# Kernel tuning notes

Measured on AMD Instinct MI355X. Metric: run time of the kernel, lower is better.

Reference implementation:

```python
import jax, jax.numpy as jnp
import numpy as np

B, S, HOPS, DIM, NREL = 1024, 32, 2, 64, 237
NENT, NEDGE = 14541, 272115
SIGMA = 0.1
CFMW = 64


def setup_inputs() -> dict:
    key = jax.random.key(0)
    ks = jax.random.split(key, 20)

    def g(k, shape):
        return (jax.random.normal(k, shape, dtype=jnp.float32) / np.float32(np.sqrt(shape[0])))

    inp = {
        "entity_pairs": jax.random.randint(ks[0], (B, 2), 0, NENT),
        "train_edges": jax.random.randint(ks[1], (B,), 0, NEDGE),
        "labels": jax.random.randint(ks[2], (B,), 0, NREL),
        "entity2edges": jax.random.randint(ks[3], (NENT + 1, S), 0, NEDGE + 1),
        "edge2entities": jax.random.randint(ks[4], (NEDGE + 1, 1), 0, NENT + 1),
        "edge2relation": jax.random.randint(ks[5], (NEDGE + 1,), 0, NREL + 1),
        "t": jax.random.uniform(ks[6], (B,), dtype=jnp.float32),
        "eps": jax.random.normal(ks[7], (B, NREL), dtype=jnp.float32),
        "rel_feat": g(ks[8], (NREL, DIM)),
        "W_agg0": g(ks[9], (DIM, DIM)), "b_agg0": jnp.zeros((DIM,), jnp.float32),
        "W_agg1": g(ks[10], (DIM, NREL)), "b_agg1": jnp.zeros((NREL,), jnp.float32),
        "W_out": g(ks[11], (2 * NREL, NREL)), "b_out": jnp.zeros((NREL,), jnp.float32),
        "mW1": g(ks[12], (NREL + 1, CFMW)), "mb1": jnp.zeros((CFMW,), jnp.float32),
        "mW2": g(ks[13], (CFMW, CFMW)), "mb2": jnp.zeros((CFMW,), jnp.float32),
        "mW3": g(ks[14], (CFMW, CFMW)), "mb3": jnp.zeros((CFMW,), jnp.float32),
        "mW4": g(ks[15], (CFMW, NREL)), "mb4": jnp.zeros((NREL,), jnp.float32),
    }
    return inp


def _side(ent, labels, train_edges, entity2edges, edge2entities, edge2relation, relf, aggs):
    # multi-hop neighbor edge gather + masks (exclude the training edge itself)
    edges_list = [labels]  # hop-0 "edges" are the relation labels
    masks = []
    for i in range(HOPS):
        if i == 0:
            ne = ent.reshape(B, 1)  # (B, 1) source entities
        else:
            ne = edge2entities[edges_list[-1].reshape(-1)].reshape(B, -1)
        nedges = entity2edges[ne.reshape(-1)].reshape(B, -1)  # (B, S**(i+1))
        edges_list.append(nedges)
        masks.append((nedges != train_edges[:, None]).astype(relf.dtype))
    # edge -> relation -> feature
    ev = [relf[edges_list[0]]]  # (B, DIM)
    for edges in edges_list[1:]:
        ev.append(relf[edge2relation[edges]])  # (B, S**h, DIM)
    # iterative mean aggregation (PathCon-style, one entity per edge)
    for i in range(HOPS):
        W, b, act, self_inc = aggs[i]
        d = W.shape[0]
        nxt = []
        for hop in range(HOPS - i):
            neigh = ev[hop + 1].reshape(B, -1, 1, S, d)
            m = masks[hop].reshape(B, -1, 1, S, 1)
            out = jnp.mean(jnp.mean(neigh * m, axis=-2), axis=-2)  # (B, S**hop, d)
            if self_inc:
                out = out + ev[hop].reshape(B, -1, d)
            nxt.append(act(out @ W + b))
        ev = nxt
    return ev[0].reshape(B, NREL)


def reference(entity_pairs, train_edges, labels, entity2edges, edge2entities,
              edge2relation, t, eps, rel_feat, W_agg0, b_agg0, W_agg1, b_agg1,
              W_out, b_out, mW1, mb1, mW2, mb2, mW3, mb3, mW4, mb4):
    relf = jnp.concatenate([rel_feat, jnp.zeros((1, DIM), rel_feat.dtype)], axis=0)
    aggs = [
        (W_agg0, b_agg0, jax.nn.relu, True),    # intermediate hop: relu, self-included
        (W_agg1, b_agg1, lambda x: x, False),   # last hop: identity, no self
    ]
    x0 = _side(entity_pairs[:, 0], labels, train_edges, entity2edges,
               edge2entities, edge2relation, relf, aggs)
    x1 = _side(entity_pairs[:, 1], labels, train_edges, entity2edges,
               edge2entities, edge2relation, relf, aggs)
    output = jnp.concatenate([x0, x1], axis=-1) @ W_out + b_out  # (B, NREL)
    # CFM: xt = (1-t) x0 + t x1 + sigma*eps ; ut = x1 - x0
    tb = t[:, None]
    xt = (1.0 - tb) * x0 + tb * x1 + SIGMA * eps
    h = jnp.concatenate([xt, tb], axis=-1)
    h = jax.nn.selu(h @ mW1 + mb1)
    h = jax.nn.selu(h @ mW2 + mb2)
    h = jax.nn.selu(h @ mW3 + mb3)
    vt = h @ mW4 + mb4
    scores = output * vt
    return scores
```

## Files before the change

kernel.cpp:

```cpp
#include <hip/hip_runtime.h>
#include <math.h>

#define BB 1024
#define S 32
#define DIM 64
#define NREL 237
#define SIGMA 0.1f

#define OFS_WR    0
#define N_WR      (238*64)
#define OFS_WC0   (OFS_WR + N_WR)
#define N_WC      (64*237)
#define OFS_WC1   (OFS_WC0 + N_WC)
#define OFS_BC    (OFS_WC1 + N_WC)
#define OFS_HC    (OFS_BC + 237)

#define LDS_BYTES 76288

__device__ __forceinline__ float selu_f(float x) {
    const float alpha = 1.6732632423543772f;
    const float scale = 1.0507009873554805f;
    return scale * (x > 0.f ? x : alpha * expm1f(x));
}

__global__ __launch_bounds__(256) void precompute_kernel(
    const float* __restrict__ rel_feat, const float* __restrict__ W0,
    const float* __restrict__ W1, const float* __restrict__ b1,
    const float* __restrict__ W_out, const float* __restrict__ b_out,
    const float* __restrict__ mW1, const float* __restrict__ mb1,
    float* __restrict__ ws) {
    __shared__ float red[256];
    int blk = blockIdx.x;
    const int tid = threadIdx.x;

    if (blk < 60) {
        int idx = blk * 256 + tid;
        if (idx < 238 * 64) {
            int r = idx >> 6, o = idx & 63;
            float acc = 0.f;
            if (r < NREL) {
#pragma unroll 8
                for (int d = 0; d < 64; ++d)
                    acc += rel_feat[r * 64 + d] * W0[d * 64 + o];
            }
            ws[OFS_WR + idx] = acc;
        }
        return;
    }
    blk -= 60;
    if (blk < 512) {
        int half = blk >> 8;
        int lb = blk & 255;
        int o = lb >> 2, ct = lb & 3;
        int cl = tid & 63, g = tid >> 6;
        int c = ct * 64 + cl;
        const float* Wsrc = W_out + half * 237 * 237;
        float acc = 0.f;
        if (c < NREL) {
            int k0 = g * 60, k1 = (g == 3) ? 237 : (k0 + 60);
#pragma unroll 4
            for (int k = k0; k < k1; ++k)
                acc += W1[o * 237 + k] * Wsrc[k * 237 + c];
        }
        red[tid] = acc;
        __syncthreads();
        if (g == 0 && c < NREL) {
            float s = red[cl] + red[64 + cl] + red[128 + cl] + red[192 + cl];
            ws[(half ? OFS_WC1 : OFS_WC0) + o * 237 + c] = s;
        }
        return;
    }
    blk -= 512;
    if (blk < 4) {
        int cl = tid & 63, g = tid >> 6;
        int c = blk * 64 + cl;
        float acc = 0.f;
        if (c < NREL) {
            int k0 = g * 60, k1 = (g == 3) ? 237 : (k0 + 60);
#pragma unroll 4
            for (int k = k0; k < k1; ++k)
                acc += b1[k] * (W_out[k * 237 + c] + W_out[(237 + k) * 237 + c]);
        }
        red[tid] = acc;
        __syncthreads();
        if (g == 0 && c < NREL)
            ws[OFS_BC + c] = b_out[c] + red[cl] + red[64 + cl] + red[128 + cl] + red[192 + cl];
        return;
    }
    {
        int w = tid & 63, g = tid >> 6;
        int k0 = g * 60, k1 = (g == 3) ? 237 : (k0 + 60);
        float acc = 0.f;
#pragma unroll 4
        for (int k = k0; k < k1; ++k)
            acc += b1[k] * mW1[k * 64 + w];
        red[tid] = acc;
        __syncthreads();
        if (g == 0)
            ws[OFS_HC + w] = mb1[w] + red[w] + red[64 + w] + red[128 + w] + red[192 + w];
    }
}

__global__ __launch_bounds__(512) void gf_kernel(
    const int* __restrict__ ep, const int* __restrict__ te_arr,
    const int* __restrict__ e2e_tab, const int* __restrict__ e2ent,
    const int* __restrict__ e2r, const float* __restrict__ b0,
    const float* __restrict__ t_arr, const float* __restrict__ eps,
    const float* __restrict__ W1, const float* __restrict__ mW1,
    const float* __restrict__ mW2, const float* __restrict__ mb2,
    const float* __restrict__ mW3, const float* __restrict__ mb3,
    const float* __restrict__ mW4, const float* __restrict__ mb4,
    const float* __restrict__ ws, float* __restrict__ out) {
    extern __shared__ float smem[];
    float* s_wr   = smem;
    int*   s_r2m  = (int*)(smem + 15232);
    int*   s_r1   = (int*)(smem + 16256);
    int*   s_ent2 = (int*)(smem + 16384);
    float* s_m1   = smem + 16512;
    float* s_v1   = smem + 16640;
    float* s_ov   = smem + 18816;

    const int tid = threadIdx.x;
    const int bb = blockIdx.x * 2;
    const int g = tid >> 4;
    const int c = tid & 15;
    const int te0 = te_arr[bb];
    const int te1 = te_arr[bb + 1];
    const float4 b0v = ((const float4*)b0)[c];

    {
        const float4* src = (const float4*)(ws + OFS_WR);
        float4* dst = (float4*)s_wr;
        for (int i = tid; i < 238 * 16; i += 512) dst[i] = src[i];
    }
    const float4* sWr4 = (const float4*)s_wr;

    if (tid < 128) {
        int u = tid >> 5, s = tid & 31;
        int b = bb + (u >> 1), side = u & 1;
        int te = (u >> 1) ? te1 : te0;
        int ent = ep[b * 2 + side];
        int e1 = e2e_tab[ent * S + s];
        s_r1[u * 32 + s] = e2r[e1];
        s_m1[u * 32 + s] = (e1 != te) ? 1.0f : 0.0f;
        s_ent2[u * 32 + s] = e2ent[e1];
    }
    __syncthreads();

    for (int p = tid; p < 1024; p += 512) {
        int j = p >> 5, s = p & 31;
        int e2 = e2e_tab[s_ent2[j] * S + s];
        s_r2m[p] = (e2 == te0) ? NREL : e2r[e2];
    }
    __syncthreads();

    const float inv = 1.0f / 32.0f;
    for (int u = 0; u < 4; ++u) {
        {
            const int j = g;
            const int* rr = &s_r2m[j * 32];
            float4 acc = sWr4[s_r1[u * 32 + j] * 16 + c];
            float4 sa = make_float4(0.f, 0.f, 0.f, 0.f);
            float4 sb = make_float4(0.f, 0.f, 0.f, 0.f);
#pragma unroll
            for (int s = 0; s < 16; ++s) {
                float4 v = sWr4[rr[s] * 16 + c];
                sa.x += v.x; sa.y += v.y; sa.z += v.z; sa.w += v.w;
            }
#pragma unroll
            for (int s = 16; s < 32; ++s) {
                float4 v = sWr4[rr[s] * 16 + c];
                sb.x += v.x; sb.y += v.y; sb.z += v.z; sb.w += v.w;
            }
            float m = s_m1[u * 32 + j];
            float4 r;
            r.x = fmaxf(acc.x + (sa.x + sb.x) * inv + b0v.x, 0.f) * m;
            r.y = fmaxf(acc.y + (sa.y + sb.y) * inv + b0v.y, 0.f) * m;
            r.z = fmaxf(acc.z + (sa.z + sb.z) * inv + b0v.z, 0.f) * m;
            r.w = fmaxf(acc.w + (sa.w + sb.w) * inv + b0v.w, 0.f) * m;
            *((float4*)&s_v1[j * 68 + c * 4]) = r;
        }
        __syncthreads();
        if (tid < 64) {
            float sum = 0.f;
#pragma unroll 8
            for (int j = 0; j < 32; ++j) sum += s_v1[j * 68 + tid];
            s_ov[u * 64 + tid] = sum * inv;
        }
        if (u < 3) {
            const int un = u + 1;
            const int te = (un >> 1) ? te1 : te0;
            for (int p = tid; p < 1024; p += 512) {
                int j = p >> 5, s = p & 31;
                int e2 = e2e_tab[s_ent2[un * 32 + j] * S + s];
                s_r2m[p] = (e2 == te) ? NREL : e2r[e2];
            }
        }
        __syncthreads();
    }

    float* s_omix = smem;
    float* s_ymix = smem + 128;
    float* s_outv = smem + 608;
    float* s_red  = smem + 1088;
    float* s_h    = smem + 1600;
    const float* Wc0 = ws + OFS_WC0;
    const float* Wc1 = ws + OFS_WC1;
    const float* bc = ws + OFS_BC;
    const float* hc = ws + OFS_HC;

    const int p  = tid >> 8;
    const int lt = tid & 255;
    const float tb = t_arr[bb + p];

    if (lt < 64) {
        float o0 = s_ov[(p * 2 + 0) * 64 + lt];
        float o1 = s_ov[(p * 2 + 1) * 64 + lt];
        s_omix[p * 64 + lt] = (1.f - tb) * o0 + tb * o1;
    }
    __syncthreads();

    if (lt < NREL) {
        float y = 0.f, a = bc[lt];
#pragma unroll 4
        for (int d = 0; d < 64; ++d) {
            y += s_omix[p * 64 + d] * W1[d * 237 + lt];
            a += s_ov[p * 128 + d] * Wc0[d * 237 + lt]
               + s_ov[p * 128 + 64 + d] * Wc1[d * 237 + lt];
        }
        s_ymix[p * 240 + lt] = y;
        s_outv[p * 240 + lt] = a;
    }
    __syncthreads();

    {
        int w = lt & 63, gg = lt >> 6;
        float a = 0.f;
        int k0 = gg * 60, k1 = (gg == 3) ? 237 : (k0 + 60);
        const float* e = eps + (bb + p) * 237;
#pragma unroll 4
        for (int k = k0; k < k1; ++k)
            a += (SIGMA * e[k] + s_ymix[p * 240 + k]) * mW1[k * 64 + w];
        s_red[p * 256 + lt] = a;
    }
    __syncthreads();
    if (lt < 64) {
        float h = hc[lt] + tb * mW1[237 * 64 + lt]
                + s_red[p * 256 + lt] + s_red[p * 256 + 64 + lt]
                + s_red[p * 256 + 128 + lt] + s_red[p * 256 + 192 + lt];
        s_h[p * 64 + lt] = selu_f(h);
    }
    __syncthreads();

    {
        int w = lt & 63, gg = lt >> 6;
        float a = 0.f;
#pragma unroll
        for (int d = gg * 16; d < gg * 16 + 16; ++d)
            a += s_h[p * 64 + d] * mW2[d * 64 + w];
        s_red[p * 256 + lt] = a;
    }
    __syncthreads();
    if (lt < 64) {
        float v = mb2[lt] + s_red[p * 256 + lt] + s_red[p * 256 + 64 + lt]
                + s_red[p * 256 + 128 + lt] + s_red[p * 256 + 192 + lt];
        s_h[p * 64 + lt] = selu_f(v);
    }
    __syncthreads();

    {
        int w = lt & 63, gg = lt >> 6;
        float a = 0.f;
#pragma unroll
        for (int d = gg * 16; d < gg * 16 + 16; ++d)
            a += s_h[p * 64 + d] * mW3[d * 64 + w];
        s_red[p * 256 + lt] = a;
    }
    __syncthreads();
    if (lt < 64) {
        float v = mb3[lt] + s_red[p * 256 + lt] + s_red[p * 256 + 64 + lt]
                + s_red[p * 256 + 128 + lt] + s_red[p * 256 + 192 + lt];
        s_h[p * 64 + lt] = selu_f(v);
    }
    __syncthreads();

    if (lt < NREL) {
        float a = mb4[lt];
#pragma unroll 4
        for (int w = 0; w < 64; ++w)
            a += s_h[p * 64 + w] * mW4[w * 237 + lt];
        out[(bb + p) * 237 + lt] = s_outv[p * 240 + lt] * a;
    }
}

extern "C" void kernel_launch(void* const* d_in, const int* in_sizes, int n_in,
                              void* d_out, int out_size, void* d_ws, size_t ws_size,
                              hipStream_t stream) {
    const int* ep       = (const int*)d_in[0];
    const int* te       = (const int*)d_in[1];
    const int* e2e      = (const int*)d_in[3];
    const int* e2ent    = (const int*)d_in[4];
    const int* e2r      = (const int*)d_in[5];
    const float* t      = (const float*)d_in[6];
    const float* eps    = (const float*)d_in[7];
    const float* relf   = (const float*)d_in[8];
    const float* W0     = (const float*)d_in[9];
    const float* b0     = (const float*)d_in[10];
    const float* W1     = (const float*)d_in[11];
    const float* b1     = (const float*)d_in[12];
    const float* W_out  = (const float*)d_in[13];
    const float* b_out  = (const float*)d_in[14];
    const float* mW1    = (const float*)d_in[15];
    const float* mb1    = (const float*)d_in[16];
    const float* mW2    = (const float*)d_in[17];
    const float* mb2    = (const float*)d_in[18];
    const float* mW3    = (const float*)d_in[19];
    const float* mb3    = (const float*)d_in[20];
    const float* mW4    = (const float*)d_in[21];
    const float* mb4    = (const float*)d_in[22];
    float* ws  = (float*)d_ws;
    float* out = (float*)d_out;

    hipLaunchKernelGGL(precompute_kernel, dim3(577), dim3(256), 0, stream,
                       relf, W0, W1, b1, W_out, b_out, mW1, mb1, ws);
    hipLaunchKernelGGL(gf_kernel, dim3(BB / 2), dim3(512), LDS_BYTES, stream,
                       ep, te, e2e, e2ent, e2r, b0,
                       t, eps, W1, mW1, mW2, mb2, mW3, mb3, mW4, mb4, ws, out);
}
```

Before: 147.5 us.

## Store relation-weight table as bf16 in LDS and process one sample per block

The precomputed relation×W0 table is now rounded to bf16, which halves its global-to-LDS copy and LDS footprint (about 44KB instead of 76KB). That allows more blocks to be resident per CU. The main kernel now runs one batch row per 512-thread block with 1024 blocks instead of two rows per block. The MLP reductions are rewritten to spread work over all 512 threads with 8-way partial sums. The cost is bf16 rounding error in the aggregated features, and each block still repeats the table load.

```diff
diff --git a/kernel.cpp b/kernel.cpp
--- a/kernel.cpp
+++ b/kernel.cpp
@@ -7,20 +7,23 @@
 #define NREL 237
 #define SIGMA 0.1f
 
-#define OFS_WR    0
-#define N_WR      (238*64)
-#define OFS_WC0   (OFS_WR + N_WR)
+#define OFS_WC0   7616
 #define N_WC      (64*237)
 #define OFS_WC1   (OFS_WC0 + N_WC)
 #define OFS_BC    (OFS_WC1 + N_WC)
 #define OFS_HC    (OFS_BC + 237)
 
-#define LDS_BYTES 76288
+#define LDS_BYTES 44544
 
 __device__ __forceinline__ float selu_f(float x) {
     const float alpha = 1.6732632423543772f;
     const float scale = 1.0507009873554805f;
     return scale * (x > 0.f ? x : alpha * expm1f(x));
+}
+
+__device__ __forceinline__ unsigned short f2bf(float f) {
+    unsigned int b = __float_as_uint(f);
+    return (unsigned short)((b + 0x7fffu + ((b >> 16) & 1u)) >> 16);
 }
 
 __global__ __launch_bounds__(256) void precompute_kernel(
@@ -43,7 +46,7 @@
                 for (int d = 0; d < 64; ++d)
                     acc += rel_feat[r * 64 + d] * W0[d * 64 + o];
             }
-            ws[OFS_WR + idx] = acc;
+            ((unsigned short*)ws)[idx] = f2bf(acc);
         }
         return;
     }
@@ -101,6 +104,12 @@
     }
 }
 
+#define BF_ACC(sum, d) {                                                  \
+    sum.x += __uint_as_float((d).x << 16);                                \
+    sum.y += __uint_as_float((d).x & 0xffff0000u);                        \
+    sum.z += __uint_as_float((d).y << 16);                                \
+    sum.w += __uint_as_float((d).y & 0xffff0000u); }
+
 __global__ __launch_bounds__(512) void gf_kernel(
     const int* __restrict__ ep, const int* __restrict__ te_arr,
     const int* __restrict__ e2e_tab, const int* __restrict__ e2ent,
@@ -112,34 +121,30 @@
     const float* __restrict__ mW4, const float* __restrict__ mb4,
     const float* __restrict__ ws, float* __restrict__ out) {
     extern __shared__ float smem[];
-    float* s_wr   = smem;
-    int*   s_r2m  = (int*)(smem + 15232);
-    int*   s_r1   = (int*)(smem + 16256);
-    int*   s_ent2 = (int*)(smem + 16384);
-    float* s_m1   = smem + 16512;
-    float* s_v1   = smem + 16640;
-    float* s_ov   = smem + 18816;
+    unsigned short* s_wr = (unsigned short*)smem;
+    int*   s_r2m  = (int*)(smem + 7616);
+    int*   s_r1   = (int*)(smem + 8640);
+    int*   s_ent2 = (int*)(smem + 8704);
+    float* s_m1   = smem + 8768;
+    float* s_v1   = smem + 8832;
+    float* s_ov   = smem + 11008;
 
     const int tid = threadIdx.x;
-    const int bb = blockIdx.x * 2;
-    const int g = tid >> 4;
+    const int b = blockIdx.x;
     const int c = tid & 15;
-    const int te0 = te_arr[bb];
-    const int te1 = te_arr[bb + 1];
+    const int te = te_arr[b];
     const float4 b0v = ((const float4*)b0)[c];
 
     {
-        const float4* src = (const float4*)(ws + OFS_WR);
-        float4* dst = (float4*)s_wr;
-        for (int i = tid; i < 238 * 16; i += 512) dst[i] = src[i];
-    }
-    const float4* sWr4 = (const float4*)s_wr;
-
-    if (tid < 128) {
+        const uint4* src = (const uint4*)ws;
+        uint4* dst = (uint4*)s_wr;
+        for (int i = tid; i < 1904; i += 512) dst[i] = src[i];
+    }
+    const uint2* W2 = (const uint2*)s_wr;
+
+    if (tid < 64) {
         int u = tid >> 5, s = tid & 31;
-        int b = bb + (u >> 1), side = u & 1;
-        int te = (u >> 1) ? te1 : te0;
-        int ent = ep[b * 2 + side];
+        int ent = ep[b * 2 + u];
         int e1 = e2e_tab[ent * S + s];
         s_r1[u * 32 + s] = e2r[e1];
         s_m1[u * 32 + s] = (e1 != te) ? 1.0f : 0.0f;
@@ -150,34 +155,36 @@
     for (int p = tid; p < 1024; p += 512) {
         int j = p >> 5, s = p & 31;
         int e2 = e2e_tab[s_ent2[j] * S + s];
-        s_r2m[p] = (e2 == te0) ? NREL : e2r[e2];
+        s_r2m[p] = (e2 == te) ? NREL : e2r[e2];
     }
     __syncthreads();
 
     const float inv = 1.0f / 32.0f;
-    for (int u = 0; u < 4; ++u) {
+    for (int u = 0; u < 2; ++u) {
         {
-            const int j = g;
+            const int j = tid >> 4;
             const int* rr = &s_r2m[j * 32];
-            float4 acc = sWr4[s_r1[u * 32 + j] * 16 + c];
+            uint2 ds = W2[s_r1[u * 32 + j] * 16 + c];
+            float4 self = make_float4(0.f, 0.f, 0.f, 0.f);
+            BF_ACC(self, ds)
             float4 sa = make_float4(0.f, 0.f, 0.f, 0.f);
             float4 sb = make_float4(0.f, 0.f, 0.f, 0.f);
 #pragma unroll
             for (int s = 0; s < 16; ++s) {
-                float4 v = sWr4[rr[s] * 16 + c];
-                sa.x += v.x; sa.y += v.y; sa.z += v.z; sa.w += v.w;
+                uint2 d = W2[rr[s] * 16 + c];
+                BF_ACC(sa, d)
             }
 #pragma unroll
             for (int s = 16; s < 32; ++s) {
-                float4 v = sWr4[rr[s] * 16 + c];
-                sb.x += v.x; sb.y += v.y; sb.z += v.z; sb.w += v.w;
+                uint2 d = W2[rr[s] * 16 + c];
+                BF_ACC(sb, d)
             }
             float m = s_m1[u * 32 + j];
             float4 r;
-            r.x = fmaxf(acc.x + (sa.x + sb.x) * inv + b0v.x, 0.f) * m;
-            r.y = fmaxf(acc.y + (sa.y + sb.y) * inv + b0v.y, 0.f) * m;
-            r.z = fmaxf(acc.z + (sa.z + sb.z) * inv + b0v.z, 0.f) * m;
-            r.w = fmaxf(acc.w + (sa.w + sb.w) * inv + b0v.w, 0.f) * m;
+            r.x = fmaxf(self.x + (sa.x + sb.x) * inv + b0v.x, 0.f) * m;
+            r.y = fmaxf(self.y + (sa.y + sb.y) * inv + b0v.y, 0.f) * m;
+            r.z = fmaxf(self.z + (sa.z + sb.z) * inv + b0v.z, 0.f) * m;
+            r.w = fmaxf(self.w + (sa.w + sb.w) * inv + b0v.w, 0.f) * m;
             *((float4*)&s_v1[j * 68 + c * 4]) = r;
         }
         __syncthreads();
@@ -187,110 +194,118 @@
             for (int j = 0; j < 32; ++j) sum += s_v1[j * 68 + tid];
             s_ov[u * 64 + tid] = sum * inv;
         }
-        if (u < 3) {
-            const int un = u + 1;
-            const int te = (un >> 1) ? te1 : te0;
+        if (u == 0) {
             for (int p = tid; p < 1024; p += 512) {
                 int j = p >> 5, s = p & 31;
-                int e2 = e2e_tab[s_ent2[un * 32 + j] * S + s];
+                int e2 = e2e_tab[s_ent2[32 + j] * S + s];
                 s_r2m[p] = (e2 == te) ? NREL : e2r[e2];
             }
         }
         __syncthreads();
     }
 
-    float* s_omix = smem;
-    float* s_ymix = smem + 128;
-    float* s_outv = smem + 608;
-    float* s_red  = smem + 1088;
-    float* s_h    = smem + 1600;
+    float* s_ymix = smem;
+    float* s_outv = smem + 240;
+    float* s_red  = smem + 480;
+    float* s_h    = smem + 992;
+    float* s_omix = smem + 1056;
+    float* s_vp   = smem + 1120;
+    const float tb = t_arr[b];
     const float* Wc0 = ws + OFS_WC0;
     const float* Wc1 = ws + OFS_WC1;
     const float* bc = ws + OFS_BC;
     const float* hc = ws + OFS_HC;
 
-    const int p  = tid >> 8;
-    const int lt = tid & 255;
-    const float tb = t_arr[bb + p];
-
-    if (lt < 64) {
-        float o0 = s_ov[(p * 2 + 0) * 64 + lt];
-        float o1 = s_ov[(p * 2 + 1) * 64 + lt];
-        s_omix[p * 64 + lt] = (1.f - tb) * o0 + tb * o1;
-    }
-    __syncthreads();
-
-    if (lt < NREL) {
-        float y = 0.f, a = bc[lt];
-#pragma unroll 4
-        for (int d = 0; d < 64; ++d) {
-            y += s_omix[p * 64 + d] * W1[d * 237 + lt];
-            a += s_ov[p * 128 + d] * Wc0[d * 237 + lt]
-               + s_ov[p * 128 + 64 + d] * Wc1[d * 237 + lt];
-        }
-        s_ymix[p * 240 + lt] = y;
-        s_outv[p * 240 + lt] = a;
-    }
-    __syncthreads();
-
-    {
-        int w = lt & 63, gg = lt >> 6;
+    if (tid < 64)
+        s_omix[tid] = (1.f - tb) * s_ov[tid] + tb * s_ov[64 + tid];
+    __syncthreads();
+
+    if (tid < 256) {
+        if (tid < NREL) {
+            float y = 0.f;
+#pragma unroll 4
+            for (int d = 0; d < 64; ++d)
+                y += s_omix[d] * W1[d * 237 + tid];
+            s_ymix[tid] = y;
+        }
+    } else {
+        int cc = tid - 256;
+        if (cc < NREL) {
+            float a = bc[cc];
+#pragma unroll 4
+            for (int d = 0; d < 64; ++d)
+                a += s_ov[d] * Wc0[d * 237 + cc] + s_ov[64 + d] * Wc1[d * 237 + cc];
+            s_outv[cc] = a;
+        }
+    }
+    __syncthreads();
+
+    {
+        int w = tid & 63, q = tid >> 6;
+        int k0 = q * 30, k1 = (q == 7) ? 237 : (k0 + 30);
+        const float* e = eps + b * 237;
         float a = 0.f;
-        int k0 = gg * 60, k1 = (gg == 3) ? 237 : (k0 + 60);
-        const float* e = eps + (bb + p) * 237;
 #pragma unroll 4
         for (int k = k0; k < k1; ++k)
-            a += (SIGMA * e[k] + s_ymix[p * 240 + k]) * mW1[k * 64 + w];
-        s_red[p * 256 + lt] = a;
-    }
-    __syncthreads();
-    if (lt < 64) {
-        float h = hc[lt] + tb * mW1[237 * 64 + lt]
-                + s_red[p * 256 + lt] + s_red[p * 256 + 64 + lt]
-                + s_red[p * 256 + 128 + lt] + s_red[p * 256 + 192 + lt];
-        s_h[p * 64 + lt] = selu_f(h);
-    }
-    __syncthreads();
-
-    {
-        int w = lt & 63, gg = lt >> 6;
+            a += (SIGMA * e[k] + s_ymix[k]) * mW1[k * 64 + w];
+        s_red[tid] = a;
+    }
+    __syncthreads();
+    if (tid < 64) {
+        float h = hc[tid] + tb * mW1[237 * 64 + tid];
+#pragma unroll
+        for (int q = 0; q < 8; ++q) h += s_red[q * 64 + tid];
+        s_h[tid] = selu_f(h);
+    }
+    __syncthreads();
+
+    {
+        int w = tid & 63, q = tid >> 6;
         float a = 0.f;
 #pragma unroll
-        for (int d = gg * 16; d < gg * 16 + 16; ++d)
-            a += s_h[p * 64 + d] * mW2[d * 64 + w];
-        s_red[p * 256 + lt] = a;
-    }
-    __syncthreads();
-    if (lt < 64) {
-        float v = mb2[lt] + s_red[p * 256 + lt] + s_red[p * 256 + 64 + lt]
-                + s_red[p * 256 + 128 + lt] + s_red[p * 256 + 192 + lt];
-        s_h[p * 64 + lt] = selu_f(v);
-    }
-    __syncthreads();
-
-    {
-        int w = lt & 63, gg = lt >> 6;
+        for (int d = q * 8; d < q * 8 + 8; ++d)
+            a += s_h[d] * mW2[d * 64 + w];
+        s_red[tid] = a;
+    }
+    __syncthreads();
+    if (tid < 64) {
+        float v = mb2[tid];
+#pragma unroll
+        for (int q = 0; q < 8; ++q) v += s_red[q * 64 + tid];
+        s_h[tid] = selu_f(v);
+    }
+    __syncthreads();
+
+    {
+        int w = tid & 63, q = tid >> 6;
         float a = 0.f;
 #pragma unroll
-        for (int d = gg * 16; d < gg * 16 + 16; ++d)
-            a += s_h[p * 64 + d] * mW3[d * 64 + w];
-        s_red[p * 256 + lt] = a;
-    }
-    __syncthreads();
-    if (lt < 64) {
-        float v = mb3[lt] + s_red[p * 256 + lt] + s_red[p * 256 + 64 + lt]
-                + s_red[p * 256 + 128 + lt] + s_red[p * 256 + 192 + lt];
-        s_h[p * 64 + lt] = selu_f(v);
-    }
-    __syncthreads();
-
-    if (lt < NREL) {
-        float a = mb4[lt];
-#pragma unroll 4
-        for (int w = 0; w < 64; ++w)
-            a += s_h[p * 64 + w] * mW4[w * 237 + lt];
-        out[(bb + p) * 237 + lt] = s_outv[p * 240 + lt] * a;
-    }
+        for (int d = q * 8; d < q * 8 + 8; ++d)
+            a += s_h[d] * mW3[d * 64 + w];
+        s_red[tid] = a;
+    }
+    __syncthreads();
+    if (tid < 64) {
+        float v = mb3[tid];
+#pragma unroll
+        for (int q = 0; q < 8; ++q) v += s_red[q * 64 + tid];
+        s_h[tid] = selu_f(v);
+    }
+    __syncthreads();
+
+    {
+        int half = tid >> 8, cc = tid & 255;
+        if (cc < NREL) {
+            float a = 0.f;
+#pragma unroll 4
+            for (int w = half * 32; w < half * 32 + 32; ++w)
+                a += s_h[w] * mW4[w * 237 + cc];
+            s_vp[half * 240 + cc] = a;
+        }
+    }
+    __syncthreads();
+    if (tid < NREL)
+        out[b * 237 + tid] = s_outv[tid] * (mb4[tid] + s_vp[tid] + s_vp[240 + tid]);
 }
 
 extern "C" void kernel_launch(void* const* d_in, const int* in_sizes, int n_in,
@@ -323,7 +338,7 @@
 
     hipLaunchKernelGGL(precompute_kernel, dim3(577), dim3(256), 0, stream,
                        relf, W0, W1, b1, W_out, b_out, mW1, mb1, ws);
-    hipLaunchKernelGGL(gf_kernel, dim3(BB / 2), dim3(512), LDS_BYTES, stream,
+    hipLaunchKernelGGL(gf_kernel, dim3(BB), dim3(512), LDS_BYTES, stream,
                        ep, te, e2e, e2ent, e2r, b0,
                        t, eps, W1, mW1, mW2, mb2, mW3, mb3, mW4, mb4, ws, out);
 }
```

New measurement: 151.2 us. +2.5%, slower.
